# Optimization experiments

Measured on AMD Instinct MI355X. Metric: run time of the kernel, lower is better.

## Reference

```python
import jax, jax.numpy as jnp
import numpy as np

N_NODES = 20000
N_EDGES = 320000
HIDDEN = 64
HEADS = 8
HEAD_DIM = HIDDEN // HEADS
K_HOPS = 2
CST = 1e-05


def setup_inputs() -> dict:
    key = jax.random.key(0)
    ks = jax.random.split(key, 12)
    s = 1.0 / np.sqrt(HIDDEN)
    inp = {
        "x": jax.random.normal(ks[0], (N_NODES, HIDDEN), dtype=jnp.float32),
        "edge_index": jax.random.randint(ks[1], (2, N_EDGES), 0, N_NODES, dtype=jnp.int64),
        "edge_feature": jnp.zeros((1,), dtype=jnp.float32),  # unused by the module
        "Wq": jax.random.uniform(ks[2], (HIDDEN, HIDDEN), jnp.float32, -s, s),
        "bq": jax.random.uniform(ks[3], (HIDDEN,), jnp.float32, -s, s),
        "Wk": jax.random.uniform(ks[4], (HIDDEN, HIDDEN), jnp.float32, -s, s),
        "bk": jax.random.uniform(ks[5], (HIDDEN,), jnp.float32, -s, s),
        "Wv": jax.random.uniform(ks[6], (HIDDEN, HIDDEN), jnp.float32, -s, s),
        "bv": jax.random.uniform(ks[7], (HIDDEN,), jnp.float32, -s, s),
        "Wo": jax.random.uniform(ks[8], (HIDDEN, HIDDEN), jnp.float32, -s, s),
        "bo": jax.random.uniform(ks[9], (HIDDEN,), jnp.float32, -s, s),
        "hopwise": jnp.ones((K_HOPS + 1,), dtype=jnp.float32),
        "headwise": jnp.zeros((HEADS, K_HOPS), dtype=jnp.float32),
    }
    return inp


def reference(x, edge_index, edge_feature, Wq, bq, Wk, bk, Wv, bv, Wo, bo, hopwise, headwise):
    N = x.shape[0]
    row, col = edge_index[0], edge_index[1]

    # symmetric normalization: deg is in-degree of col
    deg = jax.ops.segment_sum(jnp.ones_like(col, dtype=x.dtype), col, num_segments=N)
    deg_inv = jnp.where(deg > 0, deg ** -0.5, 0.0)
    norm = deg_inv[row] * deg_inv[col]  # [E]

    Q = 1.0 + jax.nn.elu(x @ Wq + bq)
    K = 1.0 + jax.nn.elu(x @ Wk + bk)
    V = (x @ Wv + bv)
    Q = Q.reshape(N, HEADS, HEAD_DIM)
    K = K.reshape(N, HEADS, HEAD_DIM)
    V = V.reshape(N, HEADS, HEAD_DIM)

    M = jnp.einsum('nhi,nhj->nhij', K, V)  # [N,H,d,d]
    hidden = V * hopwise[0]
    layerwise = jax.nn.softmax(headwise, axis=0)  # softmax over heads (dim=-2)

    for hop in range(K_HOPS):
        # scatter-add propagation: out[i] = sum_{e: col[e]=i} norm[e] * state[row[e]]
        M = jax.ops.segment_sum(norm[:, None, None, None] * M[row], col, num_segments=N)
        K = jax.ops.segment_sum(norm[:, None, None] * K[row], col, num_segments=N)
        H = jnp.einsum('nhi,nhij->nhj', Q, M)
        C = jnp.einsum('nhi,nhi->nh', Q, K)[..., None] + CST
        H = H / C
        gamma = hopwise[hop + 1] * layerwise[:, hop][:, None]  # [H,1]
        hidden = hidden + gamma * H

    hidden = hidden.reshape(N, HEADS * HEAD_DIM)
    # dropout is identity in eval mode
    return hidden @ Wo + bo
```

## Files before the change

### kernel.cpp

```cpp
#include <hip/hip_runtime.h>
#include <hip/hip_bf16.h>

typedef __hip_bfloat16 bf16;
typedef __fp16 half2_t __attribute__((ext_vector_type(2)));
typedef float floatx2 __attribute__((ext_vector_type(2)));
typedef _Float16 f16x8_t __attribute__((ext_vector_type(8)));
typedef float f32x4_t __attribute__((ext_vector_type(4)));

#define N_NODES 20000
#define N_EDGES 320000
#define CSTF 1e-5f

#if defined(__has_builtin)
#if __has_builtin(__builtin_amdgcn_cvt_pk_fp8_f32) && __has_builtin(__builtin_amdgcn_cvt_pk_f32_fp8)
#define M1FP8 1
#endif
#if __has_builtin(__builtin_amdgcn_fdot2)
#define HAVE_FDOT2 1
#endif
#endif

#ifdef M1FP8
#define M1_STRIDE 128
#define M1_LANE   2
typedef uint2 m1vec;
#else
#define M1_STRIDE 256
#define M1_LANE   4
typedef uint4 m1vec;
#endif

__device__ __forceinline__ half2_t u2h(unsigned int u) {
    union { unsigned int u; half2_t h; } c; c.u = u; return c.h;
}
__device__ __forceinline__ unsigned int pkh(float a, float b) {
    union { __fp16 h[2]; unsigned int u; } c;
    c.h[0] = (__fp16)a; c.h[1] = (__fp16)b;
    return c.u;
}
__device__ __forceinline__ float fdot2(half2_t a, half2_t b, float c) {
#ifdef HAVE_FDOT2
    return __builtin_amdgcn_fdot2(a, b, c, false);
#else
    return fmaf((float)a.x, (float)b.x, fmaf((float)a.y, (float)b.y, c));
#endif
}
__device__ __forceinline__ int rdl(int v, int lane) { return __builtin_amdgcn_readlane(v, lane); }
__device__ __forceinline__ float ldf(const void* p, int i, bool bf) {
    return bf ? __bfloat162float(((const bf16*)p)[i]) : ((const float*)p)[i];
}
__device__ __forceinline__ float bfbits(unsigned int lo16) {
    union { unsigned int u; float f; } c; c.u = lo16 << 16; return c.f;
}
__device__ __forceinline__ bool wave_is_i64(const void* ei, int e) {
    unsigned int hi = ((const unsigned int*)ei)[2 * e + 1];
    return !__any(hi != 0);
}

struct Args {
    const void *x, *ei, *Wq, *bq, *Wk, *bk, *Wv, *bv, *Wo, *bo, *hopwise, *headwise;
    void* out;
    float* Q;
    _Float16 *K0h, *Vh, *K1h;
    unsigned int* M1h;
    int* bsrc;
    float* gam;
    int *deg, *cnt;
};

__global__ __launch_bounds__(256) void k_p1(Args a) {
    const int t = threadIdx.x;
    const int e = blockIdx.x * 256 + t;
    bool i64 = wave_is_i64(a.ei, e);
    int r, c;
    if (i64) {
        r = (int)((const long long*)a.ei)[e];
        c = (int)((const long long*)a.ei)[N_EDGES + e];
    } else {
        r = ((const int*)a.ei)[e];
        c = ((const int*)a.ei)[N_EDGES + e];
    }
    int slot = atomicAdd(&a.deg[c], 1);
    if (slot < 64) a.bsrc[c * 64 + slot] = r;
    if (blockIdx.x < 64) {
        int bad = 0;
        for (int i = blockIdx.x * 256 + t; i < 40000; i += 64 * 256) {
            unsigned int w = ((const unsigned int*)a.x)[i];
            if (((w >> 7)  & 0xFFu) == 0xFFu) bad++;
            if (((w >> 23) & 0xFFu) == 0xFFu) bad++;
        }
        if (bad) atomicAdd(&a.cnt[0], bad);
    }
}

__global__ __launch_bounds__(256) void k_qkv(Args a) {
    __shared__ __align__(16) _Float16 sA[4096];
    __shared__ __align__(16) _Float16 sB[12288];
    const int t = threadIdx.x;
    const bool bf = (a.cnt[0] < 16);
    const int n0 = blockIdx.x * 64;

    if (blockIdx.x == 0 && t < 8) {
        float e0 = 0.f, e1 = 0.f;
        for (int hh = 0; hh < 8; hh++) {
            e0 += __expf(ldf(a.headwise, hh * 2 + 0, bf));
            e1 += __expf(ldf(a.headwise, hh * 2 + 1, bf));
        }
        a.gam[t]     = ldf(a.hopwise, 1, bf) * __expf(ldf(a.headwise, t * 2 + 0, bf)) / e0;
        a.gam[8 + t] = ldf(a.hopwise, 2, bf) * __expf(ldf(a.headwise, t * 2 + 1, bf)) / e1;
        if (t == 0) a.gam[16] = ldf(a.hopwise, 0, bf);
    }

    for (int i = t; i < 2048; i += 256) {
        int node = i >> 5, kp = i & 31;
        int gn = n0 + node; if (gn >= N_NODES) gn = N_NODES - 1;
        float x0, x1;
        if (bf) {
            unsigned int u = ((const unsigned int*)a.x)[gn * 32 + kp];
            x0 = bfbits(u & 0xFFFFu); x1 = bfbits(u >> 16);
        } else {
            float2 xv = ((const float2*)a.x)[gn * 32 + kp];
            x0 = xv.x; x1 = xv.y;
        }
        int byte = (node * 128 + kp * 4) ^ ((node & 7) << 4);
        *(unsigned int*)((char*)sA + byte) = pkh(x0, x1);
    }
    for (int i = t; i < 6144; i += 256) {
        int kp = i / 192, n = i % 192;
        int k = kp * 2, c = n & 63;
        const void* W = (n < 64) ? a.Wq : (n < 128) ? a.Wk : a.Wv;
        float w0 = ldf(W, k * 64 + c, bf);
        float w1 = ldf(W, (k + 1) * 64 + c, bf);
        int ct = n >> 4, kh = k >> 5, kq = (k & 31) >> 3;
        int hoff = (((ct * 2 + kh) * 64 + kq * 16 + (n & 15)) << 3) + (k & 7);
        *(unsigned int*)&sB[hoff] = pkh(w0, w1);
    }
    __syncthreads();

    const int l = t & 63, w = t >> 6;
    f16x8_t Afrag[2];
    {
        int node = w * 16 + (l & 15);
        int cb = node * 128 + ((l >> 4) * 16);
        int swz = (node & 7) << 4;
        Afrag[0] = *(const f16x8_t*)((const char*)sA + ((cb)      ^ swz));
        Afrag[1] = *(const f16x8_t*)((const char*)sA + ((cb + 64) ^ swz));
    }
    f32x4_t acc[12];
#pragma unroll
    for (int ct = 0; ct < 12; ct++) acc[ct] = (f32x4_t){0.f, 0.f, 0.f, 0.f};
#pragma unroll
    for (int kh = 0; kh < 2; kh++) {
#pragma unroll
        for (int ct = 0; ct < 12; ct++) {
            f16x8_t B = *(const f16x8_t*)&sB[((ct * 2 + kh) * 64 + l) * 8];
            acc[ct] = __builtin_amdgcn_mfma_f32_16x16x32_f16(Afrag[kh], B, acc[ct], 0, 0, 0);
        }
    }
    const int dcol = l & 15;
    float bqv[4], bkv[4], bvv[4];
#pragma unroll
    for (int ct = 0; ct < 4; ct++) {
        bqv[ct] = ldf(a.bq, ct * 16 + dcol, bf);
        bkv[ct] = ldf(a.bk, ct * 16 + dcol, bf);
        bvv[ct] = ldf(a.bv, ct * 16 + dcol, bf);
    }
    const int rbase = n0 + w * 16 + ((l >> 4) << 2);
#pragma unroll
    for (int j = 0; j < 4; j++) {
        int gn = rbase + j;
        if (gn < N_NODES) {
            int dg = a.deg[gn];
            float di = dg > 0 ? rsqrtf((float)dg) : 0.0f;
#pragma unroll
            for (int ct = 0; ct < 4; ct++) {
                float q = acc[ct][j] + bqv[ct];
                a.Q[gn * 64 + ct * 16 + dcol] = q > 0.f ? q + 1.f : __expf(q);
                float kx = acc[4 + ct][j] + bkv[ct];
                float ke = kx > 0.f ? kx + 1.f : __expf(kx);
                a.K0h[gn * 64 + ct * 16 + dcol] = (_Float16)(di * ke);
                a.Vh[gn * 64 + ct * 16 + dcol] = (_Float16)(acc[8 + ct][j] + bvv[ct]);
            }
        }
    }
}

__global__ __launch_bounds__(128) void k_hop1(Args a) {
    const int l = threadIdx.x & 63;
    const int n = blockIdx.x * 2 + (threadIdx.x >> 6);
    const int hb = l & 56;
    float acc[8] = {0, 0, 0, 0, 0, 0, 0, 0};
    float kacc = 0.0f;
    const int dg = a.deg[n];
    const int m = min(dg, 64);
    if (m > 0) {
        const int srcv = a.bsrc[n * 64 + (l < m ? l : m - 1)];
#define H1_BODY(KU, VO, KO)                                                \
    {                                                                      \
        half2_t p0 = u2h(KU.x), p1 = u2h(KU.y), p2 = u2h(KU.z), p3 = u2h(KU.w); \
        float vv = (float)VO;                                              \
        acc[0] = fmaf(vv, (float)p0.x, acc[0]); acc[1] = fmaf(vv, (float)p0.y, acc[1]); \
        acc[2] = fmaf(vv, (float)p1.x, acc[2]); acc[3] = fmaf(vv, (float)p1.y, acc[3]); \
        acc[4] = fmaf(vv, (float)p2.x, acc[4]); acc[5] = fmaf(vv, (float)p2.y, acc[5]); \
        acc[6] = fmaf(vv, (float)p3.x, acc[6]); acc[7] = fmaf(vv, (float)p3.y, acc[7]); \
        kacc += (float)KO;                                                 \
    }
        int e = 0;
        for (; e + 4 <= m; e += 4) {
            int sA = rdl(srcv, e), sB = rdl(srcv, e + 1), sC = rdl(srcv, e + 2), sD = rdl(srcv, e + 3);
            uint4 kA = *(const uint4*)(a.K0h + sA * 64 + hb);
            uint4 kB = *(const uint4*)(a.K0h + sB * 64 + hb);
            uint4 kC = *(const uint4*)(a.K0h + sC * 64 + hb);
            uint4 kD = *(const uint4*)(a.K0h + sD * 64 + hb);
            __fp16 vA = a.Vh[sA * 64 + l], vB = a.Vh[sB * 64 + l];
            __fp16 vC = a.Vh[sC * 64 + l], vD = a.Vh[sD * 64 + l];
            __fp16 oA = a.K0h[sA * 64 + l], oB = a.K0h[sB * 64 + l];
            __fp16 oC = a.K0h[sC * 64 + l], oD = a.K0h[sD * 64 + l];
            H1_BODY(kA, vA, oA)
            H1_BODY(kB, vB, oB)
            H1_BODY(kC, vC, oC)
            H1_BODY(kD, vD, oD)
        }
        for (; e < m; e++) {
            int sA = rdl(srcv, e);
            uint4 kA = *(const uint4*)(a.K0h + sA * 64 + hb);
            __fp16 vA = a.Vh[sA * 64 + l];
            __fp16 oA = a.K0h[sA * 64 + l];
            H1_BODY(kA, vA, oA)
        }
#undef H1_BODY
        float inv = 1.0f / (float)dg;
#pragma unroll
        for (int i = 0; i < 8; i++) acc[i] *= inv;
        kacc *= inv;
    }
#ifdef M1FP8
    unsigned int w0 = 0, w1 = 0;
    w0 = __builtin_amdgcn_cvt_pk_fp8_f32(acc[0], acc[1], w0, false);
    w0 = __builtin_amdgcn_cvt_pk_fp8_f32(acc[2], acc[3], w0, true);
    w1 = __builtin_amdgcn_cvt_pk_fp8_f32(acc[4], acc[5], w1, false);
    w1 = __builtin_amdgcn_cvt_pk_fp8_f32(acc[6], acc[7], w1, true);
    uint2 o2; o2.x = w0; o2.y = w1;
    *(uint2*)(a.M1h + (size_t)n * M1_STRIDE + l * M1_LANE) = o2;
#else
    uint4 o;
    o.x = pkh(acc[0], acc[1]); o.y = pkh(acc[2], acc[3]);
    o.z = pkh(acc[4], acc[5]); o.w = pkh(acc[6], acc[7]);
    *(uint4*)(a.M1h + (size_t)n * M1_STRIDE + l * M1_LANE) = o;
#endif
    a.K1h[n * 64 + l] = (_Float16)kacc;
}

__global__ __launch_bounds__(512, 4) void k_hop2o(Args a) {
    __shared__ __align__(16) _Float16 sH[1024];
    __shared__ __align__(16) _Float16 sWo[4096];
    const int t = threadIdx.x;
    const bool bf = (a.cnt[0] < 16);
    const int l = t & 63;
    const int wv = t >> 6;
    const int n = blockIdx.x * 8 + wv;
    const int hb = l & 56, h = l >> 3;

    for (int i = t; i < 2048; i += 512) {
        int kp = i >> 6, c = i & 63;
        int k = kp * 2;
        float w0 = ldf(a.Wo, k * 64 + c, bf);
        float w1 = ldf(a.Wo, (k + 1) * 64 + c, bf);
        int ct = c >> 4, kh = k >> 5, kq = (k & 31) >> 3;
        int hoff = (((ct * 2 + kh) * 64 + kq * 16 + (c & 15)) << 3) + (k & 7);
        *(unsigned int*)&sWo[hoff] = pkh(w0, w1);
    }

    const float4 qa = *(const float4*)(a.Q + n * 64 + hb);
    const float4 qb = *(const float4*)(a.Q + n * 64 + hb + 4);
    const float qown = a.Q[n * 64 + l];
    float hacc = 0.0f, sk = 0.0f;
    const int dg = a.deg[n];
    const int m = min(dg, 64);
#ifdef M1FP8
#define H2_DOT(MU, DST)                                                    \
    {                                                                      \
        floatx2 a0 = __builtin_amdgcn_cvt_pk_f32_fp8(MU.x, false);         \
        floatx2 a1 = __builtin_amdgcn_cvt_pk_f32_fp8(MU.x, true);          \
        floatx2 a2 = __builtin_amdgcn_cvt_pk_f32_fp8(MU.y, false);         \
        floatx2 a3 = __builtin_amdgcn_cvt_pk_f32_fp8(MU.y, true);          \
        DST = qa.x * a0.x;                                                 \
        DST = fmaf(qa.y, a0.y, DST); DST = fmaf(qa.z, a1.x, DST);          \
        DST = fmaf(qa.w, a1.y, DST); DST = fmaf(qb.x, a2.x, DST);          \
        DST = fmaf(qb.y, a2.y, DST); DST = fmaf(qb.z, a3.x, DST);          \
        DST = fmaf(qb.w, a3.y, DST);                                       \
    }
#else
    const half2_t q01 = u2h(pkh(qa.x, qa.y));
    const half2_t q23 = u2h(pkh(qa.z, qa.w));
    const half2_t q45 = u2h(pkh(qb.x, qb.y));
    const half2_t q67 = u2h(pkh(qb.z, qb.w));
#define H2_DOT(MU, DST)                                                    \
    {                                                                      \
        DST = fdot2(q01, u2h(MU.x), 0.0f);                                 \
        DST = fdot2(q23, u2h(MU.y), DST);                                  \
        DST = fdot2(q45, u2h(MU.z), DST);                                  \
        DST = fdot2(q67, u2h(MU.w), DST);                                  \
    }
#endif
    if (m > 0) {
        const int srcv = a.bsrc[n * 64 + (l < m ? l : m - 1)];
        int e = 0;
        for (; e + 8 <= m; e += 8) {
            int s_[8];
            m1vec m_[8];
            __fp16 k_[8];
#pragma unroll
            for (int u = 0; u < 8; u++) s_[u] = rdl(srcv, e + u);
#pragma unroll
            for (int u = 0; u < 8; u++) m_[u] = *(const m1vec*)(a.M1h + (size_t)s_[u] * M1_STRIDE + l * M1_LANE);
#pragma unroll
            for (int u = 0; u < 8; u++) k_[u] = a.K1h[s_[u] * 64 + l];
#pragma unroll
            for (int u = 0; u < 8; u++) {
                float d;
                H2_DOT(m_[u], d)
                hacc += d;
                sk += (float)k_[u];
            }
        }
        for (; e < m; e++) {
            int sA = rdl(srcv, e);
            m1vec mA = *(const m1vec*)(a.M1h + (size_t)sA * M1_STRIDE + l * M1_LANE);
            __fp16 kA = a.K1h[sA * 64 + l];
            float d;
            H2_DOT(mA, d)
            hacc += d;
            sk += (float)kA;
        }
    }
    m1vec mo = *(const m1vec*)(a.M1h + (size_t)n * M1_STRIDE + l * M1_LANE);
    float h1r;
    H2_DOT(mo, h1r)
#undef H2_DOT
    const float din = dg > 0 ? rsqrtf((float)dg) : 0.0f;
    const float sq  = dg > 0 ? sqrtf((float)dg)  : 0.0f;
    float h1 = h1r * sq;
    float c1 = qown * (float)a.K1h[n * 64 + l];
    float c2 = qown * sk;
#pragma unroll
    for (int dd = 1; dd < 8; dd <<= 1) {
        c1 += __shfl_xor(c1, dd);
        c2 += __shfl_xor(c2, dd);
    }
    c1 *= sq;
    c2 *= din;
    float H2v = hacc * din;

    float hidden = a.gam[16] * (float)a.Vh[n * 64 + l]
                 + a.gam[h] * h1 / (c1 + CSTF)
                 + a.gam[8 + h] * H2v / (c2 + CSTF);

    {
        int byte = (wv * 128 + l * 2) ^ ((wv & 7) << 4);
        *(_Float16*)((char*)sH + byte) = (_Float16)hidden;
    }
    __syncthreads();

    if (wv < 4) {
        const int ct = wv;
        int row = l & 15;
        int swz = (row & 7) << 4;
        int cb = row * 128 + ((l >> 4) * 16);
        f16x8_t A0 = *(const f16x8_t*)((const char*)sH + ((cb)      ^ swz));
        f16x8_t A1 = *(const f16x8_t*)((const char*)sH + ((cb + 64) ^ swz));
        f32x4_t acc = (f32x4_t){0.f, 0.f, 0.f, 0.f};
        f16x8_t B0 = *(const f16x8_t*)&sWo[((ct * 2 + 0) * 64 + l) * 8];
        f16x8_t B1 = *(const f16x8_t*)&sWo[((ct * 2 + 1) * 64 + l) * 8];
        acc = __builtin_amdgcn_mfma_f32_16x16x32_f16(A0, B0, acc, 0, 0, 0);
        acc = __builtin_amdgcn_mfma_f32_16x16x32_f16(A1, B1, acc, 0, 0, 0);
        const int dcol = l & 15;
        const float bov = ldf(a.bo, ct * 16 + dcol, bf);
        const int rb = (l >> 4) * 4;
        if (rb < 8) {
            const int gb = blockIdx.x * 8 + rb;
#pragma unroll
            for (int j = 0; j < 4; j++) {
                float o = acc[j] + bov;
                if (bf) ((bf16*)a.out)[(gb + j) * 64 + ct * 16 + dcol] = __float2bfloat16(o);
                else    ((float*)a.out)[(gb + j) * 64 + ct * 16 + dcol] = o;
            }
        }
    }
}

extern "C" void kernel_launch(void* const* d_in, const int* in_sizes, int n_in,
                              void* d_out, int out_size, void* d_ws, size_t ws_size,
                              hipStream_t stream) {
    char* p = (char*)d_ws;
    auto alloc = [&](size_t bytes) {
        void* r = (void*)p;
        p += (bytes + 255) & ~(size_t)255;
        return r;
    };
    Args a;
    a.x = d_in[0];  a.ei = d_in[1];
    a.Wq = d_in[3]; a.bq = d_in[4];
    a.Wk = d_in[5]; a.bk = d_in[6];
    a.Wv = d_in[7]; a.bv = d_in[8];
    a.Wo = d_in[9]; a.bo = d_in[10];
    a.hopwise = d_in[11]; a.headwise = d_in[12];
    a.out = d_out;

    a.Q    = (float*)alloc((size_t)N_NODES * 64 * 4);
    a.K0h  = (_Float16*)alloc((size_t)N_NODES * 64 * 2);
    a.Vh   = (_Float16*)alloc((size_t)N_NODES * 64 * 2);
    a.K1h  = (_Float16*)alloc((size_t)N_NODES * 64 * 2);
    a.M1h  = (unsigned int*)alloc((size_t)N_NODES * 1024);
    a.bsrc = (int*)alloc((size_t)N_NODES * 64 * 4);
    a.gam  = (float*)alloc(256);
    int* zz = (int*)alloc(((size_t)N_NODES + 64) * 4);
    a.deg = zz;
    a.cnt = zz + N_NODES;

    (void)hipMemsetAsync(zz, 0, ((size_t)N_NODES + 64) * 4, stream);

    const int EB = (N_EDGES + 255) / 256;
    const int GB = (N_NODES + 63) / 64;
    k_p1<<<EB, 256, 0, stream>>>(a);
    k_qkv<<<GB, 256, 0, stream>>>(a);
    k_hop1<<<N_NODES / 2, 128, 0, stream>>>(a);
    k_hop2o<<<N_NODES / 8, 512, 0, stream>>>(a);
}
```

Before: 174.2 us.

## Interleave K/V and M1/K1 gathers, store Q in fp16, shrink hop2 blocks

Packs K0 and V into one 32-bit word per element so hop1 does one scalar gather per source instead of two. It also interleaves the fp8 M1 state with the fp32 K1 sum into a 12-byte record, so hop2 fetches both with one uint3 load. Q is now stored as fp16 rather than fp32, which halves its traffic at a small precision cost. The hop2/output kernel moves from 8-node 512-thread blocks to 4-node 256-thread blocks so every wave does MFMA work, though the Wo staging into shared memory is now repeated across twice as many blocks.

```diff
diff --git a/kernel.cpp b/kernel.cpp
--- a/kernel.cpp
+++ b/kernel.cpp
@@ -20,16 +20,6 @@
 #endif
 #endif
 
-#ifdef M1FP8
-#define M1_STRIDE 128
-#define M1_LANE   2
-typedef uint2 m1vec;
-#else
-#define M1_STRIDE 256
-#define M1_LANE   4
-typedef uint4 m1vec;
-#endif
-
 __device__ __forceinline__ half2_t u2h(unsigned int u) {
     union { unsigned int u; half2_t h; } c; c.u = u; return c.h;
 }
@@ -60,9 +50,12 @@
 struct Args {
     const void *x, *ei, *Wq, *bq, *Wk, *bk, *Wv, *bv, *Wo, *bo, *hopwise, *headwise;
     void* out;
-    float* Q;
-    _Float16 *K0h, *Vh, *K1h;
+    _Float16* Qh;
+    _Float16* K0h;
+    unsigned int* KVh;
+    unsigned int* M1K;
     unsigned int* M1h;
+    _Float16* K1h;
     int* bsrc;
     float* gam;
     int *deg, *cnt;
@@ -126,11 +119,13 @@
         *(unsigned int*)((char*)sA + byte) = pkh(x0, x1);
     }
     for (int i = t; i < 6144; i += 256) {
-        int kp = i / 192, n = i % 192;
-        int k = kp * 2, c = n & 63;
-        const void* W = (n < 64) ? a.Wq : (n < 128) ? a.Wk : a.Wv;
+        int g = i >> 6, c = i & 63;
+        int kp = g / 3, wsel = g - kp * 3;
+        int k = kp * 2;
+        const void* W = (wsel == 0) ? a.Wq : (wsel == 1) ? a.Wk : a.Wv;
         float w0 = ldf(W, k * 64 + c, bf);
         float w1 = ldf(W, (k + 1) * 64 + c, bf);
+        int n = wsel * 64 + c;
         int ct = n >> 4, kh = k >> 5, kq = (k & 31) >> 3;
         int hoff = (((ct * 2 + kh) * 64 + kq * 16 + (n & 15)) << 3) + (k & 7);
         *(unsigned int*)&sB[hoff] = pkh(w0, w1);
@@ -175,11 +170,13 @@
 #pragma unroll
             for (int ct = 0; ct < 4; ct++) {
                 float q = acc[ct][j] + bqv[ct];
-                a.Q[gn * 64 + ct * 16 + dcol] = q > 0.f ? q + 1.f : __expf(q);
+                a.Qh[gn * 64 + ct * 16 + dcol] = (_Float16)(q > 0.f ? q + 1.f : __expf(q));
                 float kx = acc[4 + ct][j] + bkv[ct];
                 float ke = kx > 0.f ? kx + 1.f : __expf(kx);
-                a.K0h[gn * 64 + ct * 16 + dcol] = (_Float16)(di * ke);
-                a.Vh[gn * 64 + ct * 16 + dcol] = (_Float16)(acc[8 + ct][j] + bvv[ct]);
+                float k0s = di * ke;
+                float vv = acc[8 + ct][j] + bvv[ct];
+                a.K0h[gn * 64 + ct * 16 + dcol] = (_Float16)k0s;
+                a.KVh[gn * 64 + ct * 16 + dcol] = pkh(k0s, vv);
             }
         }
     }
@@ -195,15 +192,16 @@
     const int m = min(dg, 64);
     if (m > 0) {
         const int srcv = a.bsrc[n * 64 + (l < m ? l : m - 1)];
-#define H1_BODY(KU, VO, KO)                                                \
+#define H1_BODY(KU, KVU)                                                   \
     {                                                                      \
         half2_t p0 = u2h(KU.x), p1 = u2h(KU.y), p2 = u2h(KU.z), p3 = u2h(KU.w); \
-        float vv = (float)VO;                                              \
+        half2_t kv = u2h(KVU);                                             \
+        float vv = (float)kv.y;                                            \
         acc[0] = fmaf(vv, (float)p0.x, acc[0]); acc[1] = fmaf(vv, (float)p0.y, acc[1]); \
         acc[2] = fmaf(vv, (float)p1.x, acc[2]); acc[3] = fmaf(vv, (float)p1.y, acc[3]); \
         acc[4] = fmaf(vv, (float)p2.x, acc[4]); acc[5] = fmaf(vv, (float)p2.y, acc[5]); \
         acc[6] = fmaf(vv, (float)p3.x, acc[6]); acc[7] = fmaf(vv, (float)p3.y, acc[7]); \
-        kacc += (float)KO;                                                 \
+        kacc += (float)kv.x;                                               \
     }
         int e = 0;
         for (; e + 4 <= m; e += 4) {
@@ -212,21 +210,18 @@
             uint4 kB = *(const uint4*)(a.K0h + sB * 64 + hb);
             uint4 kC = *(const uint4*)(a.K0h + sC * 64 + hb);
             uint4 kD = *(const uint4*)(a.K0h + sD * 64 + hb);
-            __fp16 vA = a.Vh[sA * 64 + l], vB = a.Vh[sB * 64 + l];
-            __fp16 vC = a.Vh[sC * 64 + l], vD = a.Vh[sD * 64 + l];
-            __fp16 oA = a.K0h[sA * 64 + l], oB = a.K0h[sB * 64 + l];
-            __fp16 oC = a.K0h[sC * 64 + l], oD = a.K0h[sD * 64 + l];
-            H1_BODY(kA, vA, oA)
-            H1_BODY(kB, vB, oB)
-            H1_BODY(kC, vC, oC)
-            H1_BODY(kD, vD, oD)
+            unsigned int vA = a.KVh[sA * 64 + l], vB = a.KVh[sB * 64 + l];
+            unsigned int vC = a.KVh[sC * 64 + l], vD = a.KVh[sD * 64 + l];
+            H1_BODY(kA, vA)
+            H1_BODY(kB, vB)
+            H1_BODY(kC, vC)
+            H1_BODY(kD, vD)
         }
         for (; e < m; e++) {
             int sA = rdl(srcv, e);
             uint4 kA = *(const uint4*)(a.K0h + sA * 64 + hb);
-            __fp16 vA = a.Vh[sA * 64 + l];
-            __fp16 oA = a.K0h[sA * 64 + l];
-            H1_BODY(kA, vA, oA)
+            unsigned int vA = a.KVh[sA * 64 + l];
+            H1_BODY(kA, vA)
         }
 #undef H1_BODY
         float inv = 1.0f / (float)dg;
@@ -240,28 +235,29 @@
     w0 = __builtin_amdgcn_cvt_pk_fp8_f32(acc[2], acc[3], w0, true);
     w1 = __builtin_amdgcn_cvt_pk_fp8_f32(acc[4], acc[5], w1, false);
     w1 = __builtin_amdgcn_cvt_pk_fp8_f32(acc[6], acc[7], w1, true);
-    uint2 o2; o2.x = w0; o2.y = w1;
-    *(uint2*)(a.M1h + (size_t)n * M1_STRIDE + l * M1_LANE) = o2;
+    uint3 o3;
+    o3.x = w0; o3.y = w1; o3.z = __float_as_uint(kacc);
+    *(uint3*)(a.M1K + (size_t)n * 192 + l * 3) = o3;
 #else
     uint4 o;
     o.x = pkh(acc[0], acc[1]); o.y = pkh(acc[2], acc[3]);
     o.z = pkh(acc[4], acc[5]); o.w = pkh(acc[6], acc[7]);
-    *(uint4*)(a.M1h + (size_t)n * M1_STRIDE + l * M1_LANE) = o;
-#endif
+    *(uint4*)(a.M1h + (size_t)n * 256 + l * 4) = o;
     a.K1h[n * 64 + l] = (_Float16)kacc;
-}
-
-__global__ __launch_bounds__(512, 4) void k_hop2o(Args a) {
+#endif
+}
+
+__global__ __launch_bounds__(256, 4) void k_hop2o(Args a) {
     __shared__ __align__(16) _Float16 sH[1024];
     __shared__ __align__(16) _Float16 sWo[4096];
     const int t = threadIdx.x;
     const bool bf = (a.cnt[0] < 16);
     const int l = t & 63;
     const int wv = t >> 6;
-    const int n = blockIdx.x * 8 + wv;
+    const int n = blockIdx.x * 4 + wv;
     const int hb = l & 56, h = l >> 3;
 
-    for (int i = t; i < 2048; i += 512) {
+    for (int i = t; i < 2048; i += 256) {
         int kp = i >> 6, c = i & 63;
         int k = kp * 2;
         float w0 = ldf(a.Wo, k * 64 + c, bf);
@@ -271,30 +267,60 @@
         *(unsigned int*)&sWo[hoff] = pkh(w0, w1);
     }
 
-    const float4 qa = *(const float4*)(a.Q + n * 64 + hb);
-    const float4 qb = *(const float4*)(a.Q + n * 64 + hb + 4);
-    const float qown = a.Q[n * 64 + l];
+    const uint4 qrow = *(const uint4*)(a.Qh + n * 64 + hb);
+    const half2_t q01 = u2h(qrow.x), q23 = u2h(qrow.y), q45 = u2h(qrow.z), q67 = u2h(qrow.w);
+    const float qown = (float)a.Qh[n * 64 + l];
     float hacc = 0.0f, sk = 0.0f;
     const int dg = a.deg[n];
     const int m = min(dg, 64);
 #ifdef M1FP8
-#define H2_DOT(MU, DST)                                                    \
+    const float qf0 = (float)q01.x, qf1 = (float)q01.y, qf2 = (float)q23.x, qf3 = (float)q23.y;
+    const float qf4 = (float)q45.x, qf5 = (float)q45.y, qf6 = (float)q67.x, qf7 = (float)q67.y;
+#define H2_DOT(MX, MY, DST)                                                \
     {                                                                      \
-        floatx2 a0 = __builtin_amdgcn_cvt_pk_f32_fp8(MU.x, false);         \
-        floatx2 a1 = __builtin_amdgcn_cvt_pk_f32_fp8(MU.x, true);          \
-        floatx2 a2 = __builtin_amdgcn_cvt_pk_f32_fp8(MU.y, false);         \
-        floatx2 a3 = __builtin_amdgcn_cvt_pk_f32_fp8(MU.y, true);          \
-        DST = qa.x * a0.x;                                                 \
-        DST = fmaf(qa.y, a0.y, DST); DST = fmaf(qa.z, a1.x, DST);          \
-        DST = fmaf(qa.w, a1.y, DST); DST = fmaf(qb.x, a2.x, DST);          \
-        DST = fmaf(qb.y, a2.y, DST); DST = fmaf(qb.z, a3.x, DST);          \
-        DST = fmaf(qb.w, a3.y, DST);                                       \
-    }
+        floatx2 a0 = __builtin_amdgcn_cvt_pk_f32_fp8(MX, false);           \
+        floatx2 a1 = __builtin_amdgcn_cvt_pk_f32_fp8(MX, true);            \
+        floatx2 a2 = __builtin_amdgcn_cvt_pk_f32_fp8(MY, false);           \
+        floatx2 a3 = __builtin_amdgcn_cvt_pk_f32_fp8(MY, true);            \
+        DST = qf0 * a0.x;                                                  \
+        DST = fmaf(qf1, a0.y, DST); DST = fmaf(qf2, a1.x, DST);            \
+        DST = fmaf(qf3, a1.y, DST); DST = fmaf(qf4, a2.x, DST);            \
+        DST = fmaf(qf5, a2.y, DST); DST = fmaf(qf6, a3.x, DST);            \
+        DST = fmaf(qf7, a3.y, DST);                                        \
+    }
+    if (m > 0) {
+        const int srcv = a.bsrc[n * 64 + (l < m ? l : m - 1)];
+        int e = 0;
+        for (; e + 8 <= m; e += 8) {
+            int s_[8];
+            uint3 r_[8];
+#pragma unroll
+            for (int u = 0; u < 8; u++) s_[u] = rdl(srcv, e + u);
+#pragma unroll
+            for (int u = 0; u < 8; u++) r_[u] = *(const uint3*)(a.M1K + (size_t)s_[u] * 192 + l * 3);
+#pragma unroll
+            for (int u = 0; u < 8; u++) {
+                float d;
+                H2_DOT(r_[u].x, r_[u].y, d)
+                hacc += d;
+                sk += __uint_as_float(r_[u].z);
+            }
+        }
+        for (; e < m; e++) {
+            int sA = rdl(srcv, e);
+            uint3 rA = *(const uint3*)(a.M1K + (size_t)sA * 192 + l * 3);
+            float d;
+            H2_DOT(rA.x, rA.y, d)
+            hacc += d;
+            sk += __uint_as_float(rA.z);
+        }
+    }
+    const uint3 mo = *(const uint3*)(a.M1K + (size_t)n * 192 + l * 3);
+    float h1r;
+    H2_DOT(mo.x, mo.y, h1r)
+    const float ownK1 = __uint_as_float(mo.z);
+#undef H2_DOT
 #else
-    const half2_t q01 = u2h(pkh(qa.x, qa.y));
-    const half2_t q23 = u2h(pkh(qa.z, qa.w));
-    const half2_t q45 = u2h(pkh(qb.x, qb.y));
-    const half2_t q67 = u2h(pkh(qb.z, qb.w));
 #define H2_DOT(MU, DST)                                                    \
     {                                                                      \
         DST = fdot2(q01, u2h(MU.x), 0.0f);                                 \
@@ -302,18 +328,17 @@
         DST = fdot2(q45, u2h(MU.z), DST);                                  \
         DST = fdot2(q67, u2h(MU.w), DST);                                  \
     }
-#endif
     if (m > 0) {
         const int srcv = a.bsrc[n * 64 + (l < m ? l : m - 1)];
         int e = 0;
         for (; e + 8 <= m; e += 8) {
             int s_[8];
-            m1vec m_[8];
+            uint4 m_[8];
             __fp16 k_[8];
 #pragma unroll
             for (int u = 0; u < 8; u++) s_[u] = rdl(srcv, e + u);
 #pragma unroll
-            for (int u = 0; u < 8; u++) m_[u] = *(const m1vec*)(a.M1h + (size_t)s_[u] * M1_STRIDE + l * M1_LANE);
+            for (int u = 0; u < 8; u++) m_[u] = *(const uint4*)(a.M1h + (size_t)s_[u] * 256 + l * 4);
 #pragma unroll
             for (int u = 0; u < 8; u++) k_[u] = a.K1h[s_[u] * 64 + l];
 #pragma unroll
@@ -326,7 +351,7 @@
         }
         for (; e < m; e++) {
             int sA = rdl(srcv, e);
-            m1vec mA = *(const m1vec*)(a.M1h + (size_t)sA * M1_STRIDE + l * M1_LANE);
+            uint4 mA = *(const uint4*)(a.M1h + (size_t)sA * 256 + l * 4);
             __fp16 kA = a.K1h[sA * 64 + l];
             float d;
             H2_DOT(mA, d)
@@ -334,14 +359,16 @@
             sk += (float)kA;
         }
     }
-    m1vec mo = *(const m1vec*)(a.M1h + (size_t)n * M1_STRIDE + l * M1_LANE);
+    const uint4 mo = *(const uint4*)(a.M1h + (size_t)n * 256 + l * 4);
     float h1r;
     H2_DOT(mo, h1r)
+    const float ownK1 = (float)a.K1h[n * 64 + l];
 #undef H2_DOT
+#endif
     const float din = dg > 0 ? rsqrtf((float)dg) : 0.0f;
     const float sq  = dg > 0 ? sqrtf((float)dg)  : 0.0f;
     float h1 = h1r * sq;
-    float c1 = qown * (float)a.K1h[n * 64 + l];
+    float c1 = qown * ownK1;
     float c2 = qown * sk;
 #pragma unroll
     for (int dd = 1; dd < 8; dd <<= 1) {
@@ -352,7 +379,8 @@
     c2 *= din;
     float H2v = hacc * din;
 
-    float hidden = a.gam[16] * (float)a.Vh[n * 64 + l]
+    const float vown = (float)u2h(a.KVh[n * 64 + l]).y;
+    float hidden = a.gam[16] * vown
                  + a.gam[h] * h1 / (c1 + CSTF)
                  + a.gam[8 + h] * H2v / (c2 + CSTF);
 
@@ -362,7 +390,7 @@
     }
     __syncthreads();
 
-    if (wv < 4) {
+    {
         const int ct = wv;
         int row = l & 15;
         int swz = (row & 7) << 4;
@@ -377,8 +405,8 @@
         const int dcol = l & 15;
         const float bov = ldf(a.bo, ct * 16 + dcol, bf);
         const int rb = (l >> 4) * 4;
-        if (rb < 8) {
-            const int gb = blockIdx.x * 8 + rb;
+        if (rb < 4) {
+            const int gb = blockIdx.x * 4 + rb;
 #pragma unroll
             for (int j = 0; j < 4; j++) {
                 float o = acc[j] + bov;
@@ -407,11 +435,12 @@
     a.hopwise = d_in[11]; a.headwise = d_in[12];
     a.out = d_out;
 
-    a.Q    = (float*)alloc((size_t)N_NODES * 64 * 4);
+    a.Qh   = (_Float16*)alloc((size_t)N_NODES * 64 * 2);
     a.K0h  = (_Float16*)alloc((size_t)N_NODES * 64 * 2);
-    a.Vh   = (_Float16*)alloc((size_t)N_NODES * 64 * 2);
+    a.KVh  = (unsigned int*)alloc((size_t)N_NODES * 64 * 4);
+    a.M1K  = (unsigned int*)alloc((size_t)N_NODES * 192 * 4);
+    a.M1h  = (unsigned int*)alloc((size_t)N_NODES * 256 * 4);
     a.K1h  = (_Float16*)alloc((size_t)N_NODES * 64 * 2);
-    a.M1h  = (unsigned int*)alloc((size_t)N_NODES * 1024);
     a.bsrc = (int*)alloc((size_t)N_NODES * 64 * 4);
     a.gam  = (float*)alloc(256);
     int* zz = (int*)alloc(((size_t)N_NODES + 64) * 4);
@@ -425,5 +454,5 @@
     k_p1<<<EB, 256, 0, stream>>>(a);
     k_qkv<<<GB, 256, 0, stream>>>(a);
     k_hop1<<<N_NODES / 2, 128, 0, stream>>>(a);
-    k_hop2o<<<N_NODES / 8, 512, 0, stream>>>(a);
-}
+    k_hop2o<<<N_NODES / 4, 256, 0, stream>>>(a);
+}
```

Result: slower. 178.9 us (+2.7%).

## Store Q in fp16 and interleave K0/V into one packed gather array

Applied to the files above, without the earlier changes.

Q is now stored as fp16 rather than fp32, which halves its write and read traffic. The per-lane K0 and V values are packed together into one 32-bit KV array, so each neighbor gather in hop1 loads one dword instead of two separate halfwords. The x staging load in the QKV kernel is widened to float4/uint2, and the weight staging index order is changed. In exchange, the extra KV array adds write traffic in the QKV kernel, and the lower Q precision slightly raises numeric error.

```diff
diff --git a/kernel.cpp b/kernel.cpp
--- a/kernel.cpp
+++ b/kernel.cpp
@@ -60,9 +60,11 @@
 struct Args {
     const void *x, *ei, *Wq, *bq, *Wk, *bk, *Wv, *bv, *Wo, *bo, *hopwise, *headwise;
     void* out;
-    float* Q;
-    _Float16 *K0h, *Vh, *K1h;
+    _Float16* Qh;
+    _Float16* K0h;
+    unsigned int* KVh;
     unsigned int* M1h;
+    _Float16* K1h;
     int* bsrc;
     float* gam;
     int *deg, *cnt;
@@ -111,26 +113,30 @@
         if (t == 0) a.gam[16] = ldf(a.hopwise, 0, bf);
     }
 
-    for (int i = t; i < 2048; i += 256) {
-        int node = i >> 5, kp = i & 31;
+    for (int i = t; i < 1024; i += 256) {
+        int node = i >> 4, kp2 = i & 15;
         int gn = n0 + node; if (gn >= N_NODES) gn = N_NODES - 1;
-        float x0, x1;
+        unsigned int u0, u1;
         if (bf) {
-            unsigned int u = ((const unsigned int*)a.x)[gn * 32 + kp];
-            x0 = bfbits(u & 0xFFFFu); x1 = bfbits(u >> 16);
+            uint2 uu = ((const uint2*)a.x)[gn * 16 + kp2];
+            u0 = pkh(bfbits(uu.x & 0xFFFFu), bfbits(uu.x >> 16));
+            u1 = pkh(bfbits(uu.y & 0xFFFFu), bfbits(uu.y >> 16));
         } else {
-            float2 xv = ((const float2*)a.x)[gn * 32 + kp];
-            x0 = xv.x; x1 = xv.y;
-        }
-        int byte = (node * 128 + kp * 4) ^ ((node & 7) << 4);
-        *(unsigned int*)((char*)sA + byte) = pkh(x0, x1);
+            float4 xv = ((const float4*)a.x)[gn * 16 + kp2];
+            u0 = pkh(xv.x, xv.y); u1 = pkh(xv.z, xv.w);
+        }
+        int byte = (node * 128 + kp2 * 8) ^ ((node & 7) << 4);
+        uint2 o; o.x = u0; o.y = u1;
+        *(uint2*)((char*)sA + byte) = o;
     }
     for (int i = t; i < 6144; i += 256) {
-        int kp = i / 192, n = i % 192;
-        int k = kp * 2, c = n & 63;
-        const void* W = (n < 64) ? a.Wq : (n < 128) ? a.Wk : a.Wv;
+        int g = i >> 6, c = i & 63;
+        int kp = g / 3, wsel = g - kp * 3;
+        int k = kp * 2;
+        const void* W = (wsel == 0) ? a.Wq : (wsel == 1) ? a.Wk : a.Wv;
         float w0 = ldf(W, k * 64 + c, bf);
         float w1 = ldf(W, (k + 1) * 64 + c, bf);
+        int n = wsel * 64 + c;
         int ct = n >> 4, kh = k >> 5, kq = (k & 31) >> 3;
         int hoff = (((ct * 2 + kh) * 64 + kq * 16 + (n & 15)) << 3) + (k & 7);
         *(unsigned int*)&sB[hoff] = pkh(w0, w1);
@@ -175,11 +181,13 @@
 #pragma unroll
             for (int ct = 0; ct < 4; ct++) {
                 float q = acc[ct][j] + bqv[ct];
-                a.Q[gn * 64 + ct * 16 + dcol] = q > 0.f ? q + 1.f : __expf(q);
+                a.Qh[gn * 64 + ct * 16 + dcol] = (_Float16)(q > 0.f ? q + 1.f : __expf(q));
                 float kx = acc[4 + ct][j] + bkv[ct];
                 float ke = kx > 0.f ? kx + 1.f : __expf(kx);
-                a.K0h[gn * 64 + ct * 16 + dcol] = (_Float16)(di * ke);
-                a.Vh[gn * 64 + ct * 16 + dcol] = (_Float16)(acc[8 + ct][j] + bvv[ct]);
+                float k0s = di * ke;
+                float vv = acc[8 + ct][j] + bvv[ct];
+                a.K0h[gn * 64 + ct * 16 + dcol] = (_Float16)k0s;
+                a.KVh[gn * 64 + ct * 16 + dcol] = pkh(k0s, vv);
             }
         }
     }
@@ -195,15 +203,16 @@
     const int m = min(dg, 64);
     if (m > 0) {
         const int srcv = a.bsrc[n * 64 + (l < m ? l : m - 1)];
-#define H1_BODY(KU, VO, KO)                                                \
+#define H1_BODY(KU, KVU)                                                   \
     {                                                                      \
         half2_t p0 = u2h(KU.x), p1 = u2h(KU.y), p2 = u2h(KU.z), p3 = u2h(KU.w); \
-        float vv = (float)VO;                                              \
+        half2_t kv = u2h(KVU);                                             \
+        float vv = (float)kv.y;                                            \
         acc[0] = fmaf(vv, (float)p0.x, acc[0]); acc[1] = fmaf(vv, (float)p0.y, acc[1]); \
         acc[2] = fmaf(vv, (float)p1.x, acc[2]); acc[3] = fmaf(vv, (float)p1.y, acc[3]); \
         acc[4] = fmaf(vv, (float)p2.x, acc[4]); acc[5] = fmaf(vv, (float)p2.y, acc[5]); \
         acc[6] = fmaf(vv, (float)p3.x, acc[6]); acc[7] = fmaf(vv, (float)p3.y, acc[7]); \
-        kacc += (float)KO;                                                 \
+        kacc += (float)kv.x;                                               \
     }
         int e = 0;
         for (; e + 4 <= m; e += 4) {
@@ -212,21 +221,18 @@
             uint4 kB = *(const uint4*)(a.K0h + sB * 64 + hb);
             uint4 kC = *(const uint4*)(a.K0h + sC * 64 + hb);
             uint4 kD = *(const uint4*)(a.K0h + sD * 64 + hb);
-            __fp16 vA = a.Vh[sA * 64 + l], vB = a.Vh[sB * 64 + l];
-            __fp16 vC = a.Vh[sC * 64 + l], vD = a.Vh[sD * 64 + l];
-            __fp16 oA = a.K0h[sA * 64 + l], oB = a.K0h[sB * 64 + l];
-            __fp16 oC = a.K0h[sC * 64 + l], oD = a.K0h[sD * 64 + l];
-            H1_BODY(kA, vA, oA)
-            H1_BODY(kB, vB, oB)
-            H1_BODY(kC, vC, oC)
-            H1_BODY(kD, vD, oD)
+            unsigned int vA = a.KVh[sA * 64 + l], vB = a.KVh[sB * 64 + l];
+            unsigned int vC = a.KVh[sC * 64 + l], vD = a.KVh[sD * 64 + l];
+            H1_BODY(kA, vA)
+            H1_BODY(kB, vB)
+            H1_BODY(kC, vC)
+            H1_BODY(kD, vD)
         }
         for (; e < m; e++) {
             int sA = rdl(srcv, e);
             uint4 kA = *(const uint4*)(a.K0h + sA * 64 + hb);
-            __fp16 vA = a.Vh[sA * 64 + l];
-            __fp16 oA = a.K0h[sA * 64 + l];
-            H1_BODY(kA, vA, oA)
+            unsigned int vA = a.KVh[sA * 64 + l];
+            H1_BODY(kA, vA)
         }
 #undef H1_BODY
         float inv = 1.0f / (float)dg;
@@ -271,30 +277,28 @@
         *(unsigned int*)&sWo[hoff] = pkh(w0, w1);
     }
 
-    const float4 qa = *(const float4*)(a.Q + n * 64 + hb);
-    const float4 qb = *(const float4*)(a.Q + n * 64 + hb + 4);
-    const float qown = a.Q[n * 64 + l];
+    const uint4 qrow = *(const uint4*)(a.Qh + n * 64 + hb);
+    const half2_t q01 = u2h(qrow.x), q23 = u2h(qrow.y), q45 = u2h(qrow.z), q67 = u2h(qrow.w);
+    const float qown = (float)a.Qh[n * 64 + l];
     float hacc = 0.0f, sk = 0.0f;
     const int dg = a.deg[n];
     const int m = min(dg, 64);
 #ifdef M1FP8
+    const float qf0 = (float)q01.x, qf1 = (float)q01.y, qf2 = (float)q23.x, qf3 = (float)q23.y;
+    const float qf4 = (float)q45.x, qf5 = (float)q45.y, qf6 = (float)q67.x, qf7 = (float)q67.y;
 #define H2_DOT(MU, DST)                                                    \
     {                                                                      \
         floatx2 a0 = __builtin_amdgcn_cvt_pk_f32_fp8(MU.x, false);         \
         floatx2 a1 = __builtin_amdgcn_cvt_pk_f32_fp8(MU.x, true);          \
         floatx2 a2 = __builtin_amdgcn_cvt_pk_f32_fp8(MU.y, false);         \
         floatx2 a3 = __builtin_amdgcn_cvt_pk_f32_fp8(MU.y, true);          \
-        DST = qa.x * a0.x;                                                 \
-        DST = fmaf(qa.y, a0.y, DST); DST = fmaf(qa.z, a1.x, DST);          \
-        DST = fmaf(qa.w, a1.y, DST); DST = fmaf(qb.x, a2.x, DST);          \
-        DST = fmaf(qb.y, a2.y, DST); DST = fmaf(qb.z, a3.x, DST);          \
-        DST = fmaf(qb.w, a3.y, DST);                                       \
+        DST = qf0 * a0.x;                                                  \
+        DST = fmaf(qf1, a0.y, DST); DST = fmaf(qf2, a1.x, DST);            \
+        DST = fmaf(qf3, a1.y, DST); DST = fmaf(qf4, a2.x, DST);            \
+        DST = fmaf(qf5, a2.y, DST); DST = fmaf(qf6, a3.x, DST);            \
+        DST = fmaf(qf7, a3.y, DST);                                        \
     }
 #else
-    const half2_t q01 = u2h(pkh(qa.x, qa.y));
-    const half2_t q23 = u2h(pkh(qa.z, qa.w));
-    const half2_t q45 = u2h(pkh(qb.x, qb.y));
-    const half2_t q67 = u2h(pkh(qb.z, qb.w));
 #define H2_DOT(MU, DST)                                                    \
     {                                                                      \
         DST = fdot2(q01, u2h(MU.x), 0.0f);                                 \
@@ -338,10 +342,11 @@
     float h1r;
     H2_DOT(mo, h1r)
 #undef H2_DOT
+    const float ownK1 = (float)a.K1h[n * 64 + l];
     const float din = dg > 0 ? rsqrtf((float)dg) : 0.0f;
     const float sq  = dg > 0 ? sqrtf((float)dg)  : 0.0f;
     float h1 = h1r * sq;
-    float c1 = qown * (float)a.K1h[n * 64 + l];
+    float c1 = qown * ownK1;
     float c2 = qown * sk;
 #pragma unroll
     for (int dd = 1; dd < 8; dd <<= 1) {
@@ -352,7 +357,8 @@
     c2 *= din;
     float H2v = hacc * din;
 
-    float hidden = a.gam[16] * (float)a.Vh[n * 64 + l]
+    const float vown = (float)u2h(a.KVh[n * 64 + l]).y;
+    float hidden = a.gam[16] * vown
                  + a.gam[h] * h1 / (c1 + CSTF)
                  + a.gam[8 + h] * H2v / (c2 + CSTF);
 
@@ -407,11 +413,11 @@
     a.hopwise = d_in[11]; a.headwise = d_in[12];
     a.out = d_out;
 
-    a.Q    = (float*)alloc((size_t)N_NODES * 64 * 4);
+    a.Qh   = (_Float16*)alloc((size_t)N_NODES * 64 * 2);
     a.K0h  = (_Float16*)alloc((size_t)N_NODES * 64 * 2);
-    a.Vh   = (_Float16*)alloc((size_t)N_NODES * 64 * 2);
+    a.KVh  = (unsigned int*)alloc((size_t)N_NODES * 64 * 4);
+    a.M1h  = (unsigned int*)alloc((size_t)N_NODES * M1_STRIDE * 4);
     a.K1h  = (_Float16*)alloc((size_t)N_NODES * 64 * 2);
-    a.M1h  = (unsigned int*)alloc((size_t)N_NODES * 1024);
     a.bsrc = (int*)alloc((size_t)N_NODES * 64 * 4);
     a.gam  = (float*)alloc(256);
     int* zz = (int*)alloc(((size_t)N_NODES + 64) * 4);
```

Result: faster. 170.3 us, median of 2 (-2.2%).
